# Optimization experiments

Measured on AMD Instinct MI355X. Metric: run time of the kernel, lower is better.

## Reference

```python
import jax, jax.numpy as jnp
import numpy as np

EPS = 1e-3


def setup_inputs() -> dict:
    key = jax.random.key(0)
    k1, k2, k3, k4 = jax.random.split(key, 4)
    B, D, F = 1024, 1024, 32768
    x = jax.random.normal(k1, (B, D), jnp.float32)
    y = jax.random.normal(k2, (B, D), jnp.float32)
    xs = jax.random.normal(k3, (F, D), jnp.float32)
    xs = xs / jnp.linalg.norm(xs, axis=-1, keepdims=True)  # step() stores unit-norm atoms
    ys = jax.random.normal(k4, (F, D), jnp.float32)
    ys = ys / jnp.linalg.norm(ys, axis=-1, keepdims=True)
    return {"x": x, "y": y, "xs": xs, "ys": ys, "target_l0": 32}


def _grad_pursuit(signal, dictionary, target_l0):
    # signal: [B, V]; dictionary: [F, V]
    B = signal.shape[0]
    F = dictionary.shape[0]
    rows = jnp.arange(B)

    def step(weights, _):
        residual = signal - jnp.einsum('bf,fv->bv', weights, dictionary)  # [B, V]
        inner_products = jnp.einsum('bv,fv->bf', residual, dictionary)    # [B, F]
        idx = jnp.argmax(inner_products, axis=1)                          # [B]
        selected = (weights != 0).at[rows, idx].set(True)                 # [B, F] bool
        grad = jnp.where(selected, inner_products, jnp.zeros((), signal.dtype))
        c = jnp.einsum('bf,fv->bv', grad, dictionary)                     # [B, V]
        c_sq = jnp.sum(c * c, axis=-1)
        step_size = jnp.sum(c * residual, axis=-1) / jnp.maximum(c_sq, EPS)
        weights = jax.nn.relu(weights + step_size[:, None] * grad)
        return weights, None

    weights0 = jnp.zeros((B, F), signal.dtype)
    weights, _ = jax.lax.scan(step, weights0, None, length=target_l0)
    return jax.lax.top_k(weights, target_l0)  # (values [B,k], indices [B,k])


def _decode(indices, weights, dictionary):
    # embedding-bag sum: gather [B,k,V] atoms, weight, sum over k
    return jnp.einsum('bk,bkv->bv', weights, dictionary[indices])


def reference(x, y, xs, ys, target_l0):
    weights, indices = _grad_pursuit(x, xs, target_l0)
    x_reconstructed = _decode(indices, weights, xs)
    y_reconstructed = _decode(indices, weights, ys)
    losses = jnp.sum((y_reconstructed - y) ** 2, axis=-1)
    return weights, indices, x_reconstructed, y_reconstructed, losses
```

## Files before the change

kernel.cpp:

```cpp
#include <hip/hip_runtime.h>

#define B_ 1024
#define D_ 1024
#define F_ 32768
#define T_ 32
#define KSLOTS 32

#define LO_SCALE     2048.0f
#define LO_INV_SCALE 4.8828125e-4f

typedef _Float16 f16x8 __attribute__((ext_vector_type(8)));
typedef _Float16 f16x4 __attribute__((ext_vector_type(4)));
typedef float    f32x4 __attribute__((ext_vector_type(4)));

__device__ __forceinline__ unsigned int fkey(float f) {
    unsigned int u = __float_as_uint(f);
    return (u & 0x80000000u) ? ~u : (u | 0x80000000u);
}
__device__ __forceinline__ unsigned long long packkey(float v, unsigned int n) {
    return ((unsigned long long)fkey(v) << 32) | (unsigned long long)(0xFFFFFFFFu - n);
}

__device__ __forceinline__ void async16(const void* g, void* l) {
    __builtin_amdgcn_global_load_lds(
        (const __attribute__((address_space(1))) unsigned int*)g,
        (__attribute__((address_space(3))) unsigned int*)l, 16, 0, 0);
}

__device__ __forceinline__ f32x4 mfma16(f16x8 a, f16x8 b, f32x4 c) {
    return __builtin_amdgcn_mfma_f32_16x16x32_f16(a, b, c, 0, 0, 0);
}

__device__ __forceinline__ void fsplit(float v, _Float16& h, _Float16& l) {
    h = (_Float16)v;
    l = (_Float16)((v - (float)h) * LO_SCALE);
}

__global__ __launch_bounds__(256) void split_xs_kernel(
    const float* __restrict__ XS, _Float16* __restrict__ hi, _Float16* __restrict__ lo)
{
    const size_t i = ((size_t)blockIdx.x * 256 + threadIdx.x) * 4;
    const float4 v = *(const float4*)(XS + i);
    f16x4 hv, lv;
    _Float16 h, l;
    fsplit(v.x, h, l); hv[0] = h; lv[0] = l;
    fsplit(v.y, h, l); hv[1] = h; lv[1] = l;
    fsplit(v.z, h, l); hv[2] = h; lv[2] = l;
    fsplit(v.w, h, l); hv[3] = h; lv[3] = l;
    *(f16x4*)(hi + i) = hv;
    *(f16x4*)(lo + i) = lv;
}

__global__ __launch_bounds__(256) void init_kernel(
    const float* __restrict__ X, float* __restrict__ Rres,
    _Float16* __restrict__ Rhi, _Float16* __restrict__ Rlo,
    int* __restrict__ a_cnt, unsigned long long* __restrict__ amax)
{
    const int b = blockIdx.x, tid = threadIdx.x;
    for (int d = tid; d < D_; d += 256) {
        const float v = X[(size_t)b * D_ + d];
        Rres[(size_t)b * D_ + d] = v;
        _Float16 h, l; fsplit(v, h, l);
        Rhi[(size_t)b * D_ + d] = h;
        Rlo[(size_t)b * D_ + d] = l;
    }
    if (tid == 0) { a_cnt[b] = 0; amax[b] = 0ull; }
}

#define SPL1(H, L, I, V) { _Float16 _h; _Float16 _l; fsplit((V), _h, _l); H[I] = _h; L[I] = _l; }

template <bool PRE>
__global__ __launch_bounds__(256, 2) void gemm16_argmax_kernel(
    const _Float16* __restrict__ Ahi, const _Float16* __restrict__ Alo,
    const _Float16* __restrict__ Bhi, const _Float16* __restrict__ Blo,
    const float* __restrict__ XSf,
    unsigned long long* __restrict__ amax)
{
    __shared__ __align__(16) _Float16 As[2][128][32];
    __shared__ __align__(16) _Float16 Bs[2][128][32];
    __shared__ unsigned long long red[128][2];

    const int tid  = threadIdx.x;
    const int wid  = tid >> 6, lane = tid & 63;
    const int m0   = blockIdx.x * 128;
    const int n0   = blockIdx.y * 128;
    const int wm   = wid >> 1, wn = wid & 1;

    f32x4 acc[4][4], acc2[4][4];
#pragma unroll
    for (int i = 0; i < 4; ++i)
#pragma unroll
        for (int j = 0; j < 4; ++j) {
            acc[i][j]  = (f32x4){0.f, 0.f, 0.f, 0.f};
            acc2[i][j] = (f32x4){0.f, 0.f, 0.f, 0.f};
        }

    const int srow = wid * 32 + (lane >> 2);
    const int skof = (lane & 3) * 8;
    const _Float16* gAh = Ahi + (size_t)(m0 + srow) * D_ + skof;
    const _Float16* gAl = Alo + (size_t)(m0 + srow) * D_ + skof;
    const _Float16* gBh = nullptr;
    const _Float16* gBl = nullptr;
    const float*    gBf = nullptr;
    if constexpr (PRE) {
        gBh = Bhi + (size_t)(n0 + srow) * D_ + skof;
        gBl = Blo + (size_t)(n0 + srow) * D_ + skof;
    } else {
        gBf = XSf + (size_t)(n0 + (tid >> 1)) * D_ + (tid & 1) * 16;
    }

    const int lrow = lane & 15;
    const int lk   = (lane >> 4) * 8;

    for (int k0 = 0; k0 < D_; k0 += 32) {
        float4 q0, q1, q2, q3;
        if constexpr (!PRE) {
            q0 = *(const float4*)(gBf + k0);
            q1 = *(const float4*)(gBf + k0 + 4);
            q2 = *(const float4*)(gBf + k0 + 8);
            q3 = *(const float4*)(gBf + k0 + 12);
        }
        __syncthreads();
#pragma unroll
        for (int c = 0; c < 2; ++c) {
            const int ro = c * 16;
            async16(gAh + k0 + (size_t)ro * D_, &As[0][wid * 32 + ro][0]);
            async16(gAl + k0 + (size_t)ro * D_, &As[1][wid * 32 + ro][0]);
            if constexpr (PRE) {
                async16(gBh + k0 + (size_t)ro * D_, &Bs[0][wid * 32 + ro][0]);
                async16(gBl + k0 + (size_t)ro * D_, &Bs[1][wid * 32 + ro][0]);
            }
        }
        if constexpr (!PRE) {
            const int br = tid >> 1, bq = (tid & 1) * 16;
            f16x8 h0, l0, h1, l1;
            SPL1(h0, l0, 0, q0.x) SPL1(h0, l0, 1, q0.y) SPL1(h0, l0, 2, q0.z) SPL1(h0, l0, 3, q0.w)
            SPL1(h0, l0, 4, q1.x) SPL1(h0, l0, 5, q1.y) SPL1(h0, l0, 6, q1.z) SPL1(h0, l0, 7, q1.w)
            SPL1(h1, l1, 0, q2.x) SPL1(h1, l1, 1, q2.y) SPL1(h1, l1, 2, q2.z) SPL1(h1, l1, 3, q2.w)
            SPL1(h1, l1, 4, q3.x) SPL1(h1, l1, 5, q3.y) SPL1(h1, l1, 6, q3.z) SPL1(h1, l1, 7, q3.w)
            *(f16x8*)&Bs[0][br][bq]     = h0;
            *(f16x8*)&Bs[0][br][bq + 8] = h1;
            *(f16x8*)&Bs[1][br][bq]     = l0;
            *(f16x8*)&Bs[1][br][bq + 8] = l1;
        }
        __syncthreads();

        f16x8 ah[4], al[4], bh[4], bl[4];
#pragma unroll
        for (int i = 0; i < 4; ++i) {
            ah[i] = *(const f16x8*)&As[0][wm * 64 + i * 16 + lrow][lk];
            al[i] = *(const f16x8*)&As[1][wm * 64 + i * 16 + lrow][lk];
            bh[i] = *(const f16x8*)&Bs[0][wn * 64 + i * 16 + lrow][lk];
            bl[i] = *(const f16x8*)&Bs[1][wn * 64 + i * 16 + lrow][lk];
        }
#pragma unroll
        for (int i = 0; i < 4; ++i)
#pragma unroll
            for (int j = 0; j < 4; ++j) {
                acc[i][j]  = mfma16(ah[i], bh[j], acc[i][j]);
                acc2[i][j] = mfma16(ah[i], bl[j], acc2[i][j]);
                acc2[i][j] = mfma16(al[i], bh[j], acc2[i][j]);
            }
    }

    const unsigned cb = (unsigned)(n0 + wn * 64 + (lane & 15));
#pragma unroll
    for (int mi = 0; mi < 4; ++mi) {
#pragma unroll
        for (int r = 0; r < 4; ++r) {
            unsigned long long best = 0ull;
#pragma unroll
            for (int j = 0; j < 4; ++j) {
                const float v = acc[mi][j][r] + acc2[mi][j][r] * LO_INV_SCALE;
                const unsigned long long key = packkey(v, cb + (unsigned)(j * 16));
                best = key > best ? key : best;
            }
#pragma unroll
            for (int off = 1; off < 16; off <<= 1) {
                const unsigned long long o = __shfl_xor(best, off);
                best = o > best ? o : best;
            }
            if ((lane & 15) == 0)
                red[wm * 64 + mi * 16 + ((lane >> 4) << 2) + r][wn] = best;
        }
    }
    __syncthreads();
    if (tid < 128) {
        const unsigned long long b0 = red[tid][0], b1 = red[tid][1];
        atomicMax(&amax[m0 + tid], b0 > b1 ? b0 : b1);
    }
}

__global__ __launch_bounds__(256) void update_kernel(
    const float* __restrict__ X, const float* __restrict__ XS,
    float* __restrict__ Rres,
    _Float16* __restrict__ Rhi, _Float16* __restrict__ Rlo,
    int* __restrict__ a_idx, float* __restrict__ a_w, int* __restrict__ a_cnt,
    unsigned long long* __restrict__ amax)
{
    const int b = blockIdx.x;
    const int tid = threadIdx.x;
    __shared__ float s_r[D_];
    __shared__ int   s_idx[33];
    __shared__ float s_w[33];
    __shared__ float s_g[33];
    __shared__ int   s_cnt;
    __shared__ float s_red[8];

    for (int d = tid; d < D_; d += 256) s_r[d] = Rres[(size_t)b * D_ + d];

    if (tid == 0) {
        int cnt = a_cnt[b];
        for (int j = 0; j < cnt; ++j) { s_idx[j] = a_idx[b*KSLOTS + j]; s_w[j] = a_w[b*KSLOTS + j]; }
        unsigned long long key = amax[b];
        int ni = (int)(0xFFFFFFFFu - (unsigned int)(key & 0xFFFFFFFFull));
        bool found = false;
        for (int j = 0; j < cnt; ++j) found = found || (s_idx[j] == ni);
        if (!found) {
            int p = cnt;
            while (p > 0 && s_idx[p-1] > ni) { s_idx[p] = s_idx[p-1]; s_w[p] = s_w[p-1]; --p; }
            s_idx[p] = ni; s_w[p] = 0.f; ++cnt;
        }
        s_cnt = cnt;
    }
    __syncthreads();
    const int cnt = s_cnt;
    const int wave = tid >> 6, lane = tid & 63;

    for (int j = wave; j < cnt; j += 4) {
        const float* xr = XS + (size_t)s_idx[j] * D_;
        float sum = 0.f;
#pragma unroll
        for (int i = 0; i < D_/64; ++i) { int d = lane + (i << 6); sum = fmaf(s_r[d], xr[d], sum); }
        for (int off = 32; off > 0; off >>= 1) sum += __shfl_down(sum, off);
        if (lane == 0) s_g[j] = sum;
    }
    __syncthreads();

    float cs = 0.f, cr = 0.f;
#pragma unroll
    for (int v = 0; v < 4; ++v) {
        const int d = tid + (v << 8);
        float cv = 0.f;
        for (int j = 0; j < cnt; ++j) cv = fmaf(s_g[j], XS[(size_t)s_idx[j]*D_ + d], cv);
        cs = fmaf(cv, cv, cs);
        cr = fmaf(cv, s_r[d], cr);
    }
    for (int off = 32; off > 0; off >>= 1) { cs += __shfl_down(cs, off); cr += __shfl_down(cr, off); }
    if (lane == 0) { s_red[wave] = cs; s_red[4 + wave] = cr; }
    __syncthreads();

    if (tid == 0) {
        const float cs_t = s_red[0] + s_red[1] + s_red[2] + s_red[3];
        const float cr_t = s_red[4] + s_red[5] + s_red[6] + s_red[7];
        const float ss = cr_t / fmaxf(cs_t, 1e-3f);
        int nc = 0;
        for (int j = 0; j < cnt; ++j) {
            float nw = s_w[j] + ss * s_g[j];
            if (nw > 0.f) { s_idx[nc] = s_idx[j]; s_w[nc] = nw; ++nc; }
        }
        s_cnt = nc;
        a_cnt[b] = nc;
        for (int j = 0; j < nc; ++j) { a_idx[b*KSLOTS + j] = s_idx[j]; a_w[b*KSLOTS + j] = s_w[j]; }
        amax[b] = 0ull;
    }
    __syncthreads();
    const int nc = s_cnt;

#pragma unroll
    for (int v = 0; v < 4; ++v) {
        const int d = tid + (v << 8);
        float s = 0.f;
        for (int j = 0; j < nc; ++j) s = fmaf(s_w[j], XS[(size_t)s_idx[j]*D_ + d], s);
        const float rv = X[(size_t)b*D_ + d] - s;
        Rres[(size_t)b*D_ + d] = rv;
        _Float16 h, l; fsplit(rv, h, l);
        Rhi[(size_t)b*D_ + d] = h;
        Rlo[(size_t)b*D_ + d] = l;
    }
}

__global__ __launch_bounds__(256) void finalize_kernel(
    const float* __restrict__ Y,
    const float* __restrict__ XS, const float* __restrict__ YS,
    const int* __restrict__ a_idx, const float* __restrict__ a_w, const int* __restrict__ a_cnt,
    float* __restrict__ out)
{
    const int b = blockIdx.x, tid = threadIdx.x;
    __shared__ int   s_idx[KSLOTS];
    __shared__ float s_w[KSLOTS];
    __shared__ int   o_idx[KSLOTS];
    __shared__ float o_w[KSLOTS];
    __shared__ float s_red[4];

    if (tid == 0) {
        int cnt = a_cnt[b];
        for (int j = 0; j < cnt; ++j) { s_idx[j] = a_idx[b*KSLOTS + j]; s_w[j] = a_w[b*KSLOTS + j]; }
        for (int i = 1; i < cnt; ++i) {
            int ii = s_idx[i]; float ww = s_w[i];
            int p = i - 1;
            while (p >= 0 && (s_w[p] < ww || (s_w[p] == ww && s_idx[p] > ii))) {
                s_w[p+1] = s_w[p]; s_idx[p+1] = s_idx[p]; --p;
            }
            s_w[p+1] = ww; s_idx[p+1] = ii;
        }
        for (int j = 0; j < cnt; ++j) { o_idx[j] = s_idx[j]; o_w[j] = s_w[j]; }
        int p = cnt, f = 0;
        while (p < KSLOTS) {
            bool member = false;
            for (int j = 0; j < cnt; ++j) member = member || (s_idx[j] == f);
            if (!member) { o_idx[p] = f; o_w[p] = 0.f; ++p; }
            ++f;
        }
    }
    __syncthreads();

    if (tid < KSLOTS) {
        out[(size_t)b*KSLOTS + tid] = o_w[tid];
        out[32768 + (size_t)b*KSLOTS + tid] = (float)o_idx[tid];
    }

    float lsum = 0.f;
    for (int d = tid; d < D_; d += 256) {
        float xr = 0.f, yr = 0.f;
#pragma unroll
        for (int k = 0; k < KSLOTS; ++k) {
            const size_t off = (size_t)o_idx[k] * D_ + d;
            xr = fmaf(o_w[k], XS[off], xr);
            yr = fmaf(o_w[k], YS[off], yr);
        }
        out[65536 + (size_t)b*D_ + d] = xr;
        out[65536 + 1048576 + (size_t)b*D_ + d] = yr;
        const float e = yr - Y[(size_t)b*D_ + d];
        lsum = fmaf(e, e, lsum);
    }
    const int wave = tid >> 6, lane = tid & 63;
    for (int off = 32; off > 0; off >>= 1) lsum += __shfl_down(lsum, off);
    if (lane == 0) s_red[wave] = lsum;
    __syncthreads();
    if (tid == 0) out[65536 + 2097152 + b] = s_red[0] + s_red[1] + s_red[2] + s_red[3];
}

extern "C" void kernel_launch(void* const* d_in, const int* in_sizes, int n_in,
                              void* d_out, int out_size, void* d_ws, size_t ws_size,
                              hipStream_t stream) {
    (void)in_sizes; (void)n_in; (void)out_size;
    const float* x  = (const float*)d_in[0];
    const float* y  = (const float*)d_in[1];
    const float* xs = (const float*)d_in[2];
    const float* ys = (const float*)d_in[3];
    float* out = (float*)d_out;

    char* ws = (char*)d_ws;
    float*              Rres  = (float*)(ws);
    _Float16*           Rhi   = (_Float16*)(ws + ((size_t)4 << 20));
    _Float16*           Rlo   = (_Float16*)(ws + ((size_t)6 << 20));
    unsigned long long* amax  = (unsigned long long*)(ws + ((size_t)8 << 20));
    int*                a_cnt = (int*)(ws + ((size_t)8 << 20) + 8192);
    int*                a_idx = (int*)(ws + ((size_t)8 << 20) + 8192 + 4096);
    float*              a_w   = (float*)(ws + ((size_t)8 << 20) + 8192 + 4096 + 131072);
    _Float16*           XShi  = (_Float16*)(ws + ((size_t)16 << 20));
    _Float16*           XSlo  = (_Float16*)(ws + ((size_t)80 << 20));
    const bool big = ws_size >= ((size_t)144 << 20);

    if (big) split_xs_kernel<<<(F_ * D_) / 1024, 256, 0, stream>>>(xs, XShi, XSlo);
    init_kernel<<<B_, 256, 0, stream>>>(x, Rres, Rhi, Rlo, a_cnt, amax);

    dim3 ggrid(B_/128, F_/128);
    for (int t = 0; t < T_; ++t) {
        if (big)
            gemm16_argmax_kernel<true ><<<ggrid, 256, 0, stream>>>(Rhi, Rlo, XShi, XSlo, xs, amax);
        else
            gemm16_argmax_kernel<false><<<ggrid, 256, 0, stream>>>(Rhi, Rlo, nullptr, nullptr, xs, amax);
        update_kernel<<<B_, 256, 0, stream>>>(x, xs, Rres, Rhi, Rlo, a_idx, a_w, a_cnt, amax);
    }
    finalize_kernel<<<B_, 256, 0, stream>>>(y, xs, ys, a_idx, a_w, a_cnt, out);
}
```

Before: 8.575 ms.

## Double-buffer LDS tiles and remap GEMM grid for XCD-aware locality

Converts the split-fp16 GEMM+argmax kernel's K loop to double-buffered shared memory, issuing the next tile's async loads before computing the current one. This removes one barrier per step and overlaps global-to-LDS transfers with MFMA work. The grid also becomes 1D and is remapped so consecutive workgroups on the same XCD share dictionary column tiles, which should improve L2 reuse. The cost is twice the LDS per block (64KB plus reduction scratch), which may lower occupancy under launch_bounds(256,2).

```diff
diff --git a/kernel.cpp b/kernel.cpp
--- a/kernel.cpp
+++ b/kernel.cpp
@@ -76,14 +76,16 @@
     const float* __restrict__ XSf,
     unsigned long long* __restrict__ amax)
 {
-    __shared__ __align__(16) _Float16 As[2][128][32];
-    __shared__ __align__(16) _Float16 Bs[2][128][32];
+    __shared__ __align__(16) _Float16 As[2][2][128][32];
+    __shared__ __align__(16) _Float16 Bs[2][2][128][32];
     __shared__ unsigned long long red[128][2];
 
     const int tid  = threadIdx.x;
     const int wid  = tid >> 6, lane = tid & 63;
-    const int m0   = blockIdx.x * 128;
-    const int n0   = blockIdx.y * 128;
+    const int orig = (int)blockIdx.x;
+    const int wgid = (orig & 7) * 256 + (orig >> 3);
+    const int m0   = (wgid & 7) * 128;
+    const int n0   = (wgid >> 3) * 128;
     const int wm   = wid >> 1, wn = wid & 1;
 
     f32x4 acc[4][4], acc2[4][4];
@@ -112,46 +114,53 @@
     const int lrow = lane & 15;
     const int lk   = (lane >> 4) * 8;
 
-    for (int k0 = 0; k0 < D_; k0 += 32) {
-        float4 q0, q1, q2, q3;
-        if constexpr (!PRE) {
-            q0 = *(const float4*)(gBf + k0);
-            q1 = *(const float4*)(gBf + k0 + 4);
-            q2 = *(const float4*)(gBf + k0 + 8);
-            q3 = *(const float4*)(gBf + k0 + 12);
-        }
-        __syncthreads();
+    auto stageAB = [&](int bb, int k0) {
 #pragma unroll
         for (int c = 0; c < 2; ++c) {
-            const int ro = c * 16;
-            async16(gAh + k0 + (size_t)ro * D_, &As[0][wid * 32 + ro][0]);
-            async16(gAl + k0 + (size_t)ro * D_, &As[1][wid * 32 + ro][0]);
-            if constexpr (PRE) {
-                async16(gBh + k0 + (size_t)ro * D_, &Bs[0][wid * 32 + ro][0]);
-                async16(gBl + k0 + (size_t)ro * D_, &Bs[1][wid * 32 + ro][0]);
-            }
-        }
-        if constexpr (!PRE) {
-            const int br = tid >> 1, bq = (tid & 1) * 16;
-            f16x8 h0, l0, h1, l1;
-            SPL1(h0, l0, 0, q0.x) SPL1(h0, l0, 1, q0.y) SPL1(h0, l0, 2, q0.z) SPL1(h0, l0, 3, q0.w)
-            SPL1(h0, l0, 4, q1.x) SPL1(h0, l0, 5, q1.y) SPL1(h0, l0, 6, q1.z) SPL1(h0, l0, 7, q1.w)
-            SPL1(h1, l1, 0, q2.x) SPL1(h1, l1, 1, q2.y) SPL1(h1, l1, 2, q2.z) SPL1(h1, l1, 3, q2.w)
-            SPL1(h1, l1, 4, q3.x) SPL1(h1, l1, 5, q3.y) SPL1(h1, l1, 6, q3.z) SPL1(h1, l1, 7, q3.w)
-            *(f16x8*)&Bs[0][br][bq]     = h0;
-            *(f16x8*)&Bs[0][br][bq + 8] = h1;
-            *(f16x8*)&Bs[1][br][bq]     = l0;
-            *(f16x8*)&Bs[1][br][bq + 8] = l1;
-        }
-        __syncthreads();
-
+            const size_t go = (size_t)(c * 16) * D_ + k0;
+            const int    ro = wid * 32 + c * 16;
+            async16(gAh + go, &As[bb][0][ro][0]);
+            async16(gAl + go, &As[bb][1][ro][0]);
+            async16(gBh + go, &Bs[bb][0][ro][0]);
+            async16(gBl + go, &Bs[bb][1][ro][0]);
+        }
+    };
+    auto stageA = [&](int bb, int k0) {
+#pragma unroll
+        for (int c = 0; c < 2; ++c) {
+            const size_t go = (size_t)(c * 16) * D_ + k0;
+            const int    ro = wid * 32 + c * 16;
+            async16(gAh + go, &As[bb][0][ro][0]);
+            async16(gAl + go, &As[bb][1][ro][0]);
+        }
+    };
+    float4 q0, q1, q2, q3;
+    auto loadB = [&](int k0) {
+        q0 = *(const float4*)(gBf + k0);
+        q1 = *(const float4*)(gBf + k0 + 4);
+        q2 = *(const float4*)(gBf + k0 + 8);
+        q3 = *(const float4*)(gBf + k0 + 12);
+    };
+    auto writeB = [&](int bb) {
+        const int br = tid >> 1, bq = (tid & 1) * 16;
+        f16x8 h0, l0, h1, l1;
+        SPL1(h0, l0, 0, q0.x) SPL1(h0, l0, 1, q0.y) SPL1(h0, l0, 2, q0.z) SPL1(h0, l0, 3, q0.w)
+        SPL1(h0, l0, 4, q1.x) SPL1(h0, l0, 5, q1.y) SPL1(h0, l0, 6, q1.z) SPL1(h0, l0, 7, q1.w)
+        SPL1(h1, l1, 0, q2.x) SPL1(h1, l1, 1, q2.y) SPL1(h1, l1, 2, q2.z) SPL1(h1, l1, 3, q2.w)
+        SPL1(h1, l1, 4, q3.x) SPL1(h1, l1, 5, q3.y) SPL1(h1, l1, 6, q3.z) SPL1(h1, l1, 7, q3.w)
+        *(f16x8*)&Bs[bb][0][br][bq]     = h0;
+        *(f16x8*)&Bs[bb][0][br][bq + 8] = h1;
+        *(f16x8*)&Bs[bb][1][br][bq]     = l0;
+        *(f16x8*)&Bs[bb][1][br][bq + 8] = l1;
+    };
+    auto compute = [&](int bb) {
         f16x8 ah[4], al[4], bh[4], bl[4];
 #pragma unroll
         for (int i = 0; i < 4; ++i) {
-            ah[i] = *(const f16x8*)&As[0][wm * 64 + i * 16 + lrow][lk];
-            al[i] = *(const f16x8*)&As[1][wm * 64 + i * 16 + lrow][lk];
-            bh[i] = *(const f16x8*)&Bs[0][wn * 64 + i * 16 + lrow][lk];
-            bl[i] = *(const f16x8*)&Bs[1][wn * 64 + i * 16 + lrow][lk];
+            ah[i] = *(const f16x8*)&As[bb][0][wm * 64 + i * 16 + lrow][lk];
+            al[i] = *(const f16x8*)&As[bb][1][wm * 64 + i * 16 + lrow][lk];
+            bh[i] = *(const f16x8*)&Bs[bb][0][wn * 64 + i * 16 + lrow][lk];
+            bl[i] = *(const f16x8*)&Bs[bb][1][wn * 64 + i * 16 + lrow][lk];
         }
 #pragma unroll
         for (int i = 0; i < 4; ++i)
@@ -161,6 +170,34 @@
                 acc2[i][j] = mfma16(ah[i], bl[j], acc2[i][j]);
                 acc2[i][j] = mfma16(al[i], bh[j], acc2[i][j]);
             }
+    };
+
+    if constexpr (PRE) {
+        stageAB(0, 0);
+    } else {
+        loadB(0); stageA(0, 0); writeB(0);
+    }
+    __syncthreads();
+
+    for (int k0 = 0; k0 < D_; k0 += 64) {
+        if constexpr (PRE) {
+            if (k0 + 32 < D_) stageAB(1, k0 + 32);
+            compute(0);
+        } else {
+            if (k0 + 32 < D_) { loadB(k0 + 32); stageA(1, k0 + 32); }
+            compute(0);
+            if (k0 + 32 < D_) writeB(1);
+        }
+        __syncthreads();
+        if constexpr (PRE) {
+            if (k0 + 64 < D_) stageAB(0, k0 + 64);
+            compute(1);
+        } else {
+            if (k0 + 64 < D_) { loadB(k0 + 64); stageA(0, k0 + 64); }
+            compute(1);
+            if (k0 + 64 < D_) writeB(0);
+        }
+        __syncthreads();
     }
 
     const unsigned cb = (unsigned)(n0 + wn * 64 + (lane & 15));
@@ -366,12 +403,11 @@
     if (big) split_xs_kernel<<<(F_ * D_) / 1024, 256, 0, stream>>>(xs, XShi, XSlo);
     init_kernel<<<B_, 256, 0, stream>>>(x, Rres, Rhi, Rlo, a_cnt, amax);
 
-    dim3 ggrid(B_/128, F_/128);
     for (int t = 0; t < T_; ++t) {
         if (big)
-            gemm16_argmax_kernel<true ><<<ggrid, 256, 0, stream>>>(Rhi, Rlo, XShi, XSlo, xs, amax);
+            gemm16_argmax_kernel<true ><<<dim3(2048), 256, 0, stream>>>(Rhi, Rlo, XShi, XSlo, xs, amax);
         else
-            gemm16_argmax_kernel<false><<<ggrid, 256, 0, stream>>>(Rhi, Rlo, nullptr, nullptr, xs, amax);
+            gemm16_argmax_kernel<false><<<dim3(2048), 256, 0, stream>>>(Rhi, Rlo, nullptr, nullptr, xs, amax);
         update_kernel<<<B_, 256, 0, stream>>>(x, xs, Rres, Rhi, Rlo, a_idx, a_w, a_cnt, amax);
     }
     finalize_kernel<<<B_, 256, 0, stream>>>(y, xs, ys, a_idx, a_w, a_cnt, out);
```

Result: faster. 8.160 ms (-4.8%).
